# Optimization experiments

Hardware: AMD Instinct MI355X
Metric: run time of the kernel (lower is better)

The kernel has to match this reference:

```python
import jax, jax.numpy as jnp
import numpy as np

N = 100000      # nodes
E = 1600000     # edges (avg degree 16)
FEAT = 128
HID = 64
OUT = 64
NIDX = 10000
P_DROP = 0.5


def setup_inputs() -> dict:
    key = jax.random.key(0)
    ks = jax.random.split(key, 10)
    x = jax.random.normal(ks[0], (N, FEAT), jnp.float32)
    row = jax.random.randint(ks[1], (E,), 0, N)
    col = jax.random.randint(ks[2], (E,), 0, N)
    # precomputed symmetric-normalized adjacency values (D^-1/2 A D^-1/2)
    vals = jax.random.uniform(ks[3], (E,), jnp.float32) / 16.0
    W1 = jax.random.normal(ks[4], (FEAT, HID), jnp.float32) / np.sqrt(FEAT)
    b1 = jnp.zeros((HID,), jnp.float32)
    W2 = jax.random.normal(ks[5], (HID, OUT), jnp.float32) / np.sqrt(HID)
    b2 = jnp.zeros((OUT,), jnp.float32)
    # inverted-dropout mask, precomputed for determinism
    drop_mask = (jax.random.uniform(ks[6], (N, HID)) > P_DROP).astype(jnp.float32) / (1.0 - P_DROP)
    idx = jax.random.randint(ks[7], (NIDX,), 0, N)
    return dict(x=x, vals=vals, W1=W1, b1=b1, W2=W2, b2=b2,
                drop_mask=drop_mask, row=row, col=col, idx=idx)


def spmm(vals, row, col, x):
    # out[r] = sum_e vals[e] * x[col[e]] for edges with row[e]==r
    return jax.ops.segment_sum(vals[:, None] * x[col], row, num_segments=N)


def reference(x, vals, W1, b1, W2, b2, drop_mask, row, col, idx):
    h = spmm(vals, row, col, x @ W1 + b1)          # GCNConv 1: linear then A_hat @ h
    h = jax.nn.relu(h) * drop_mask                  # relu + dropout
    h = spmm(vals, row, col, h @ W2 + b2)          # GCNConv 2
    return h[idx]
```

## Files before the change

### kernel.cpp

```cpp
#include <hip/hip_runtime.h>
#include <hip/hip_bf16.h>

#define FEAT 128
#define HID  64
#define OUT  64


__global__ void scatter_direct(const int* __restrict__ row, const int* __restrict__ col,
                               const float* __restrict__ vals, int* __restrict__ cursor,
                               int2* __restrict__ edges, int E, int maxdeg) {
    int e = blockIdx.x * blockDim.x + threadIdx.x;
    if (e >= E) return;
    int r = row[e];
    int p = atomicAdd(&cursor[r], 1);
    if (p < maxdeg) {
        int2 d;
        d.x = col[e];
        d.y = __float_as_int(vals[e]);
        edges[(size_t)r * maxdeg + p] = d;
    }
}


__global__ __launch_bounds__(256) void gemm1(const float* __restrict__ x,
                                             const float* __restrict__ W1,
                                             const float* __restrict__ b1,
                                             float* __restrict__ h0, int N) {
    __shared__ float W1s[FEAT][HID];
    __shared__ float b1s[HID];
    int t = threadIdx.x;
    for (int i = t; i < FEAT * HID / 4; i += 256)
        ((float4*)&W1s[0][0])[i] = ((const float4*)W1)[i];
    if (t < HID) b1s[t] = b1[t];
    __syncthreads();

    int wave = t >> 6, lane = t & 63;
    int nquad = N >> 2;
    for (int q = blockIdx.x * 4 + wave; q < nquad; q += gridDim.x * 4) {
        int r0 = q * 4;
        const float4* x0 = (const float4*)(x + (size_t)(r0 + 0) * FEAT);
        const float4* x1 = (const float4*)(x + (size_t)(r0 + 1) * FEAT);
        const float4* x2 = (const float4*)(x + (size_t)(r0 + 2) * FEAT);
        const float4* x3 = (const float4*)(x + (size_t)(r0 + 3) * FEAT);
        float bb = b1s[lane];
        float a0 = bb, a1 = bb, a2 = bb, a3 = bb;
        #pragma unroll
        for (int k4 = 0; k4 < FEAT / 4; ++k4) {
            float w0 = W1s[k4 * 4 + 0][lane];
            float w1 = W1s[k4 * 4 + 1][lane];
            float w2 = W1s[k4 * 4 + 2][lane];
            float w3 = W1s[k4 * 4 + 3][lane];
            float4 v0 = x0[k4], v1 = x1[k4], v2 = x2[k4], v3 = x3[k4];
            a0 += v0.x * w0 + v0.y * w1 + v0.z * w2 + v0.w * w3;
            a1 += v1.x * w0 + v1.y * w1 + v1.z * w2 + v1.w * w3;
            a2 += v2.x * w0 + v2.y * w1 + v2.z * w2 + v2.w * w3;
            a3 += v3.x * w0 + v3.y * w1 + v3.z * w2 + v3.w * w3;
        }
        h0[(size_t)(r0 + 0) * HID + lane] = a0;
        h0[(size_t)(r0 + 1) * HID + lane] = a1;
        h0[(size_t)(r0 + 2) * HID + lane] = a2;
        h0[(size_t)(r0 + 3) * HID + lane] = a3;
    }
}


__device__ inline float gather_row(const float* __restrict__ feat,
                                   const int2* __restrict__ ed,
                                   int beg, int end, int lane) {
    float acc = 0.f;
    int e = beg;
    for (; e + 8 <= end; e += 8) {
        int4 p0 = *(const int4*)(ed + e);
        int4 p1 = *(const int4*)(ed + e + 2);
        int4 p2 = *(const int4*)(ed + e + 4);
        int4 p3 = *(const int4*)(ed + e + 6);
        float g0 = feat[(size_t)p0.x * HID + lane];
        float g1 = feat[(size_t)p0.z * HID + lane];
        float g2 = feat[(size_t)p1.x * HID + lane];
        float g3 = feat[(size_t)p1.z * HID + lane];
        float g4 = feat[(size_t)p2.x * HID + lane];
        float g5 = feat[(size_t)p2.z * HID + lane];
        float g6 = feat[(size_t)p3.x * HID + lane];
        float g7 = feat[(size_t)p3.z * HID + lane];
        acc += __int_as_float(p0.y) * g0; acc += __int_as_float(p0.w) * g1;
        acc += __int_as_float(p1.y) * g2; acc += __int_as_float(p1.w) * g3;
        acc += __int_as_float(p2.y) * g4; acc += __int_as_float(p2.w) * g5;
        acc += __int_as_float(p3.y) * g6; acc += __int_as_float(p3.w) * g7;
    }
    for (; e + 2 <= end; e += 2) {
        int4 p = *(const int4*)(ed + e);
        float g0 = feat[(size_t)p.x * HID + lane];
        float g1 = feat[(size_t)p.z * HID + lane];
        acc += __int_as_float(p.y) * g0; acc += __int_as_float(p.w) * g1;
    }
    if (e < end) {
        int2 p = ed[e];
        acc += __int_as_float(p.y) * feat[(size_t)p.x * HID + lane];
    }
    return acc;
}

__device__ inline float gather_row_sum(const float* __restrict__ feat,
                                       const int2* __restrict__ ed,
                                       int beg, int end, int lane, float& vsum) {
    float acc = 0.f, s = 0.f;
    int e = beg;
    for (; e + 8 <= end; e += 8) {
        int4 p0 = *(const int4*)(ed + e);
        int4 p1 = *(const int4*)(ed + e + 2);
        int4 p2 = *(const int4*)(ed + e + 4);
        int4 p3 = *(const int4*)(ed + e + 6);
        float g0 = feat[(size_t)p0.x * HID + lane];
        float g1 = feat[(size_t)p0.z * HID + lane];
        float g2 = feat[(size_t)p1.x * HID + lane];
        float g3 = feat[(size_t)p1.z * HID + lane];
        float g4 = feat[(size_t)p2.x * HID + lane];
        float g5 = feat[(size_t)p2.z * HID + lane];
        float g6 = feat[(size_t)p3.x * HID + lane];
        float g7 = feat[(size_t)p3.z * HID + lane];
        acc += __int_as_float(p0.y) * g0; acc += __int_as_float(p0.w) * g1;
        acc += __int_as_float(p1.y) * g2; acc += __int_as_float(p1.w) * g3;
        acc += __int_as_float(p2.y) * g4; acc += __int_as_float(p2.w) * g5;
        acc += __int_as_float(p3.y) * g6; acc += __int_as_float(p3.w) * g7;
        s += __int_as_float(p0.y) + __int_as_float(p0.w);
        s += __int_as_float(p1.y) + __int_as_float(p1.w);
        s += __int_as_float(p2.y) + __int_as_float(p2.w);
        s += __int_as_float(p3.y) + __int_as_float(p3.w);
    }
    for (; e + 2 <= end; e += 2) {
        int4 p = *(const int4*)(ed + e);
        float g0 = feat[(size_t)p.x * HID + lane];
        float g1 = feat[(size_t)p.z * HID + lane];
        acc += __int_as_float(p.y) * g0; acc += __int_as_float(p.w) * g1;
        s += __int_as_float(p.y) + __int_as_float(p.w);
    }
    if (e < end) {
        int2 p = ed[e];
        acc += __int_as_float(p.y) * feat[(size_t)p.x * HID + lane];
        s += __int_as_float(p.y);
    }
    vsum = s;
    return acc;
}


__global__ __launch_bounds__(256) void spmm1_relu(const float* __restrict__ h0,
                                                  const int* __restrict__ cursor,
                                                  const int2* __restrict__ edges,
                                                  const float* __restrict__ mask,
                                                  float* __restrict__ h2,
                                                  int N, int maxdeg) {
    int t = threadIdx.x, wave = t >> 6, lane = t & 63;
    for (int r = blockIdx.x * 4 + wave; r < N; r += gridDim.x * 4) {
        int deg = min(cursor[r], maxdeg);
        int beg = r * maxdeg;
        float mk = mask[(size_t)r * HID + lane];
        float acc = gather_row(h0, edges, beg, beg + deg, lane);
        h2[(size_t)r * HID + lane] = fmaxf(acc, 0.f) * mk;
    }
}


__global__ __launch_bounds__(256) void spmm2_gemm2(const float* __restrict__ h2,
                                                   const int* __restrict__ cursor,
                                                   const int2* __restrict__ edges,
                                                   const int* __restrict__ idx,
                                                   const float* __restrict__ W2,
                                                   const float* __restrict__ b2,
                                                   float* __restrict__ out,
                                                   int NIDX, int maxdeg) {
    __shared__ float W2s[HID][OUT];
    __shared__ float b2s[OUT];
    __shared__ float gs[4][HID];
    int t = threadIdx.x;
    for (int i = t; i < HID * OUT / 4; i += 256)
        ((float4*)&W2s[0][0])[i] = ((const float4*)W2)[i];
    if (t < OUT) b2s[t] = b2[t];
    __syncthreads();

    int wave = t >> 6, lane = t & 63;
    int i = blockIdx.x * 4 + wave;
    if (i >= NIDX) return;
    int r = idx[i];
    int deg = min(cursor[r], maxdeg);
    int beg = r * maxdeg;
    float vsum;
    float g = gather_row_sum(h2, edges, beg, beg + deg, lane, vsum);
    gs[wave][lane] = g;
    float o = vsum * b2s[lane];
    #pragma unroll
    for (int f = 0; f < HID; ++f)
        o += gs[wave][f] * W2s[f][lane];
    out[(size_t)i * OUT + lane] = o;
}


extern "C" void kernel_launch(void* const* d_in, const int* in_sizes, int n_in,
                              void* d_out, int out_size, void* d_ws, size_t ws_size,
                              hipStream_t stream) {
    const float* x    = (const float*)d_in[0];
    const float* vals = (const float*)d_in[1];
    const float* W1   = (const float*)d_in[2];
    const float* b1   = (const float*)d_in[3];
    const float* W2   = (const float*)d_in[4];
    const float* b2   = (const float*)d_in[5];
    const float* mask = (const float*)d_in[6];
    const int*   row  = (const int*)d_in[7];
    const int*   col  = (const int*)d_in[8];
    const int*   idx  = (const int*)d_in[9];
    float* out = (float*)d_out;

    const int N    = in_sizes[0] / FEAT;
    const int E    = in_sizes[1];
    const int NIDX = in_sizes[9];

    auto need = [&](int md) {
        return (size_t)N * HID * 4 + 256
             + (size_t)N * HID * 4 + 256
             + (size_t)N * 4 + 256
             + (size_t)N * md * 8 + 256;
    };
    int maxdeg = 48;
    while (maxdeg > 32 && need(maxdeg) > ws_size) maxdeg -= 4;

    char* ws = (char*)d_ws;
    size_t off = 0;
    auto alloc = [&](size_t bytes) { void* p = ws + off; off = (off + bytes + 255) & ~(size_t)255; return p; };
    float* h0     = (float*)alloc((size_t)N * HID * 4);
    float* h2     = (float*)alloc((size_t)N * HID * 4);
    int*   cursor = (int*)  alloc((size_t)N * 4);
    int2*  edges  = (int2*) alloc((size_t)N * maxdeg * 8);

    hipMemsetAsync(cursor, 0, (size_t)N * 4, stream);

    scatter_direct<<<(E + 255) / 256, 256, 0, stream>>>(row, col, vals, cursor, edges, E, maxdeg);
    gemm1<<<1024, 256, 0, stream>>>(x, W1, b1, h0, N);
    spmm1_relu<<<4096, 256, 0, stream>>>(h0, cursor, edges, mask, h2, N, maxdeg);
    spmm2_gemm2<<<(NIDX + 3) / 4, 256, 0, stream>>>(h2, cursor, edges, idx, W2, b2, out, NIDX, maxdeg);
}
```

Before: 408.9 us.

## Fuse edge scatter with GEMM1 and pad edge rows to process pairs of rows

Edge bucketing and the first linear layer now run in one launch, with even blocks doing the atomic scatter and odd blocks doing a shared-memory-tiled x@W1. The edge buffer is zero-filled so the SpMM loops can step in fixed groups of 8 padded edges without tail handling, and spmm1 has each wave handle two rows at once for more memory-level parallelism. This adds a memset of the whole padded edge buffer and wasted gathers on padding entries, which read node 0 with weight zero.

Measured after the change: 548.6 us. 1.34x slower.

```diff
diff --git a/kernel.cpp b/kernel.cpp
--- a/kernel.cpp
+++ b/kernel.cpp
@@ -4,143 +4,86 @@
 #define FEAT 128
 #define HID  64
 #define OUT  64
-
-
-__global__ void scatter_direct(const int* __restrict__ row, const int* __restrict__ col,
-                               const float* __restrict__ vals, int* __restrict__ cursor,
-                               int2* __restrict__ edges, int E, int maxdeg) {
-    int e = blockIdx.x * blockDim.x + threadIdx.x;
-    if (e >= E) return;
-    int r = row[e];
-    int p = atomicAdd(&cursor[r], 1);
-    if (p < maxdeg) {
-        int2 d;
-        d.x = col[e];
-        d.y = __float_as_int(vals[e]);
-        edges[(size_t)r * maxdeg + p] = d;
-    }
-}
-
-
-__global__ __launch_bounds__(256) void gemm1(const float* __restrict__ x,
-                                             const float* __restrict__ W1,
-                                             const float* __restrict__ b1,
-                                             float* __restrict__ h0, int N) {
+#define NTILE 16
+
+
+__global__ __launch_bounds__(256) void fused_scatter_gemm1(
+        const int* __restrict__ row, const int* __restrict__ col,
+        const float* __restrict__ vals, int* __restrict__ cursor,
+        int2* __restrict__ edges, int E, int maxdeg,
+        const float* __restrict__ x, const float* __restrict__ W1,
+        const float* __restrict__ b1, float* __restrict__ h0, int N,
+        int halfGrid) {
     __shared__ float W1s[FEAT][HID];
     __shared__ float b1s[HID];
+    __shared__ float xs[NTILE][FEAT];
     int t = threadIdx.x;
-    for (int i = t; i < FEAT * HID / 4; i += 256)
-        ((float4*)&W1s[0][0])[i] = ((const float4*)W1)[i];
-    if (t < HID) b1s[t] = b1[t];
-    __syncthreads();
-
-    int wave = t >> 6, lane = t & 63;
-    int nquad = N >> 2;
-    for (int q = blockIdx.x * 4 + wave; q < nquad; q += gridDim.x * 4) {
-        int r0 = q * 4;
-        const float4* x0 = (const float4*)(x + (size_t)(r0 + 0) * FEAT);
-        const float4* x1 = (const float4*)(x + (size_t)(r0 + 1) * FEAT);
-        const float4* x2 = (const float4*)(x + (size_t)(r0 + 2) * FEAT);
-        const float4* x3 = (const float4*)(x + (size_t)(r0 + 3) * FEAT);
-        float bb = b1s[lane];
-        float a0 = bb, a1 = bb, a2 = bb, a3 = bb;
-        #pragma unroll
-        for (int k4 = 0; k4 < FEAT / 4; ++k4) {
-            float w0 = W1s[k4 * 4 + 0][lane];
-            float w1 = W1s[k4 * 4 + 1][lane];
-            float w2 = W1s[k4 * 4 + 2][lane];
-            float w3 = W1s[k4 * 4 + 3][lane];
-            float4 v0 = x0[k4], v1 = x1[k4], v2 = x2[k4], v3 = x3[k4];
-            a0 += v0.x * w0 + v0.y * w1 + v0.z * w2 + v0.w * w3;
-            a1 += v1.x * w0 + v1.y * w1 + v1.z * w2 + v1.w * w3;
-            a2 += v2.x * w0 + v2.y * w1 + v2.z * w2 + v2.w * w3;
-            a3 += v3.x * w0 + v3.y * w1 + v3.z * w2 + v3.w * w3;
+    int bid = blockIdx.x;
+
+    if ((bid & 1) == 0) {
+        int tid = (bid >> 1) * 256 + t;
+        int S = halfGrid * 256;
+        int e0 = tid, e1 = tid + S, e2 = tid + 2 * S;
+        bool v0 = e0 < E, v1 = e1 < E, v2 = e2 < E;
+        int r0 = v0 ? row[e0] : 0;
+        int r1 = v1 ? row[e1] : 0;
+        int r2 = v2 ? row[e2] : 0;
+        int p0 = v0 ? atomicAdd(&cursor[r0], 1) : 0;
+        int p1 = v1 ? atomicAdd(&cursor[r1], 1) : 0;
+        int p2 = v2 ? atomicAdd(&cursor[r2], 1) : 0;
+        if (v0 && p0 < maxdeg)
+            edges[(size_t)r0 * maxdeg + p0] = make_int2(col[e0], __float_as_int(vals[e0]));
+        if (v1 && p1 < maxdeg)
+            edges[(size_t)r1 * maxdeg + p1] = make_int2(col[e1], __float_as_int(vals[e1]));
+        if (v2 && p2 < maxdeg)
+            edges[(size_t)r2 * maxdeg + p2] = make_int2(col[e2], __float_as_int(vals[e2]));
+        for (int e = tid + 3 * S; e < E; e += S) {
+            int r = row[e];
+            int p = atomicAdd(&cursor[r], 1);
+            if (p < maxdeg)
+                edges[(size_t)r * maxdeg + p] = make_int2(col[e], __float_as_int(vals[e]));
         }
-        h0[(size_t)(r0 + 0) * HID + lane] = a0;
-        h0[(size_t)(r0 + 1) * HID + lane] = a1;
-        h0[(size_t)(r0 + 2) * HID + lane] = a2;
-        h0[(size_t)(r0 + 3) * HID + lane] = a3;
+    } else {
+        for (int i = t; i < FEAT * HID / 4; i += 256)
+            ((float4*)&W1s[0][0])[i] = ((const float4*)W1)[i];
+        if (t < HID) b1s[t] = b1[t];
+        __syncthreads();
+        int wave = t >> 6, lane = t & 63;
+        int ntile = (N + NTILE - 1) / NTILE;
+        for (int tile = bid >> 1; tile < ntile; tile += halfGrid) {
+            int base = tile * NTILE;
+            float4* xs4 = (float4*)&xs[0][0];
+            const float4* xg = (const float4*)(x + (size_t)base * FEAT);
+            int lim = min(N - base, NTILE) * (FEAT / 4);
+            float4 z; z.x = z.y = z.z = z.w = 0.f;
+            xs4[t]       = (t < lim)       ? xg[t]       : z;
+            xs4[t + 256] = (t + 256 < lim) ? xg[t + 256] : z;
+            __syncthreads();
+            int r0 = base + wave * 4;
+            float bb = b1s[lane];
+            float a0 = bb, a1 = bb, a2 = bb, a3 = bb;
+            #pragma unroll
+            for (int k4 = 0; k4 < FEAT / 4; ++k4) {
+                float w0 = W1s[k4 * 4 + 0][lane];
+                float w1 = W1s[k4 * 4 + 1][lane];
+                float w2 = W1s[k4 * 4 + 2][lane];
+                float w3 = W1s[k4 * 4 + 3][lane];
+                float4 v0 = ((const float4*)xs[wave * 4 + 0])[k4];
+                float4 v1 = ((const float4*)xs[wave * 4 + 1])[k4];
+                float4 v2 = ((const float4*)xs[wave * 4 + 2])[k4];
+                float4 v3 = ((const float4*)xs[wave * 4 + 3])[k4];
+                a0 += v0.x * w0 + v0.y * w1 + v0.z * w2 + v0.w * w3;
+                a1 += v1.x * w0 + v1.y * w1 + v1.z * w2 + v1.w * w3;
+                a2 += v2.x * w0 + v2.y * w1 + v2.z * w2 + v2.w * w3;
+                a3 += v3.x * w0 + v3.y * w1 + v3.z * w2 + v3.w * w3;
+            }
+            if (r0 + 0 < N) h0[(size_t)(r0 + 0) * HID + lane] = a0;
+            if (r0 + 1 < N) h0[(size_t)(r0 + 1) * HID + lane] = a1;
+            if (r0 + 2 < N) h0[(size_t)(r0 + 2) * HID + lane] = a2;
+            if (r0 + 3 < N) h0[(size_t)(r0 + 3) * HID + lane] = a3;
+            __syncthreads();
+        }
     }
-}
-
-
-__device__ inline float gather_row(const float* __restrict__ feat,
-                                   const int2* __restrict__ ed,
-                                   int beg, int end, int lane) {
-    float acc = 0.f;
-    int e = beg;
-    for (; e + 8 <= end; e += 8) {
-        int4 p0 = *(const int4*)(ed + e);
-        int4 p1 = *(const int4*)(ed + e + 2);
-        int4 p2 = *(const int4*)(ed + e + 4);
-        int4 p3 = *(const int4*)(ed + e + 6);
-        float g0 = feat[(size_t)p0.x * HID + lane];
-        float g1 = feat[(size_t)p0.z * HID + lane];
-        float g2 = feat[(size_t)p1.x * HID + lane];
-        float g3 = feat[(size_t)p1.z * HID + lane];
-        float g4 = feat[(size_t)p2.x * HID + lane];
-        float g5 = feat[(size_t)p2.z * HID + lane];
-        float g6 = feat[(size_t)p3.x * HID + lane];
-        float g7 = feat[(size_t)p3.z * HID + lane];
-        acc += __int_as_float(p0.y) * g0; acc += __int_as_float(p0.w) * g1;
-        acc += __int_as_float(p1.y) * g2; acc += __int_as_float(p1.w) * g3;
-        acc += __int_as_float(p2.y) * g4; acc += __int_as_float(p2.w) * g5;
-        acc += __int_as_float(p3.y) * g6; acc += __int_as_float(p3.w) * g7;
-    }
-    for (; e + 2 <= end; e += 2) {
-        int4 p = *(const int4*)(ed + e);
-        float g0 = feat[(size_t)p.x * HID + lane];
-        float g1 = feat[(size_t)p.z * HID + lane];
-        acc += __int_as_float(p.y) * g0; acc += __int_as_float(p.w) * g1;
-    }
-    if (e < end) {
-        int2 p = ed[e];
-        acc += __int_as_float(p.y) * feat[(size_t)p.x * HID + lane];
-    }
-    return acc;
-}
-
-__device__ inline float gather_row_sum(const float* __restrict__ feat,
-                                       const int2* __restrict__ ed,
-                                       int beg, int end, int lane, float& vsum) {
-    float acc = 0.f, s = 0.f;
-    int e = beg;
-    for (; e + 8 <= end; e += 8) {
-        int4 p0 = *(const int4*)(ed + e);
-        int4 p1 = *(const int4*)(ed + e + 2);
-        int4 p2 = *(const int4*)(ed + e + 4);
-        int4 p3 = *(const int4*)(ed + e + 6);
-        float g0 = feat[(size_t)p0.x * HID + lane];
-        float g1 = feat[(size_t)p0.z * HID + lane];
-        float g2 = feat[(size_t)p1.x * HID + lane];
-        float g3 = feat[(size_t)p1.z * HID + lane];
-        float g4 = feat[(size_t)p2.x * HID + lane];
-        float g5 = feat[(size_t)p2.z * HID + lane];
-        float g6 = feat[(size_t)p3.x * HID + lane];
-        float g7 = feat[(size_t)p3.z * HID + lane];
-        acc += __int_as_float(p0.y) * g0; acc += __int_as_float(p0.w) * g1;
-        acc += __int_as_float(p1.y) * g2; acc += __int_as_float(p1.w) * g3;
-        acc += __int_as_float(p2.y) * g4; acc += __int_as_float(p2.w) * g5;
-        acc += __int_as_float(p3.y) * g6; acc += __int_as_float(p3.w) * g7;
-        s += __int_as_float(p0.y) + __int_as_float(p0.w);
-        s += __int_as_float(p1.y) + __int_as_float(p1.w);
-        s += __int_as_float(p2.y) + __int_as_float(p2.w);
-        s += __int_as_float(p3.y) + __int_as_float(p3.w);
-    }
-    for (; e + 2 <= end; e += 2) {
-        int4 p = *(const int4*)(ed + e);
-        float g0 = feat[(size_t)p.x * HID + lane];
-        float g1 = feat[(size_t)p.z * HID + lane];
-        acc += __int_as_float(p.y) * g0; acc += __int_as_float(p.w) * g1;
-        s += __int_as_float(p.y) + __int_as_float(p.w);
-    }
-    if (e < end) {
-        int2 p = ed[e];
-        acc += __int_as_float(p.y) * feat[(size_t)p.x * HID + lane];
-        s += __int_as_float(p.y);
-    }
-    vsum = s;
-    return acc;
 }
 
 
@@ -151,12 +94,49 @@
                                                   float* __restrict__ h2,
                                                   int N, int maxdeg) {
     int t = threadIdx.x, wave = t >> 6, lane = t & 63;
-    for (int r = blockIdx.x * 4 + wave; r < N; r += gridDim.x * 4) {
-        int deg = min(cursor[r], maxdeg);
-        int beg = r * maxdeg;
-        float mk = mask[(size_t)r * HID + lane];
-        float acc = gather_row(h0, edges, beg, beg + deg, lane);
-        h2[(size_t)r * HID + lane] = fmaxf(acc, 0.f) * mk;
+    int npair = (N + 1) >> 1;
+    for (int g = blockIdx.x * 4 + wave; g < npair; g += gridDim.x * 4) {
+        int rA = 2 * g, rB = 2 * g + 1;
+        bool vB = rB < N;
+        int degA = min(cursor[rA], maxdeg);
+        int degB = vB ? min(cursor[rB], maxdeg) : 0;
+        int nA = (degA + 7) >> 3, nB = (degB + 7) >> 3;
+        int n = max(nA, nB);
+        const int4* qA = (const int4*)(edges + (size_t)rA * maxdeg);
+        const int4* qB = (const int4*)(edges + (size_t)(vB ? rB : rA) * maxdeg);
+        float mkA = mask[(size_t)rA * HID + lane];
+        float mkB = vB ? mask[(size_t)rB * HID + lane] : 0.f;
+        float accA = 0.f, accB = 0.f;
+        for (int i = 0; i < n; ++i) {
+            int4 A0 = qA[i * 4 + 0], A1 = qA[i * 4 + 1], A2 = qA[i * 4 + 2], A3 = qA[i * 4 + 3];
+            int4 B0 = qB[i * 4 + 0], B1 = qB[i * 4 + 1], B2 = qB[i * 4 + 2], B3 = qB[i * 4 + 3];
+            float gA0 = h0[(size_t)A0.x * HID + lane];
+            float gA1 = h0[(size_t)A0.z * HID + lane];
+            float gA2 = h0[(size_t)A1.x * HID + lane];
+            float gA3 = h0[(size_t)A1.z * HID + lane];
+            float gA4 = h0[(size_t)A2.x * HID + lane];
+            float gA5 = h0[(size_t)A2.z * HID + lane];
+            float gA6 = h0[(size_t)A3.x * HID + lane];
+            float gA7 = h0[(size_t)A3.z * HID + lane];
+            float gB0 = h0[(size_t)B0.x * HID + lane];
+            float gB1 = h0[(size_t)B0.z * HID + lane];
+            float gB2 = h0[(size_t)B1.x * HID + lane];
+            float gB3 = h0[(size_t)B1.z * HID + lane];
+            float gB4 = h0[(size_t)B2.x * HID + lane];
+            float gB5 = h0[(size_t)B2.z * HID + lane];
+            float gB6 = h0[(size_t)B3.x * HID + lane];
+            float gB7 = h0[(size_t)B3.z * HID + lane];
+            accA += __int_as_float(A0.y) * gA0; accA += __int_as_float(A0.w) * gA1;
+            accA += __int_as_float(A1.y) * gA2; accA += __int_as_float(A1.w) * gA3;
+            accA += __int_as_float(A2.y) * gA4; accA += __int_as_float(A2.w) * gA5;
+            accA += __int_as_float(A3.y) * gA6; accA += __int_as_float(A3.w) * gA7;
+            accB += __int_as_float(B0.y) * gB0; accB += __int_as_float(B0.w) * gB1;
+            accB += __int_as_float(B1.y) * gB2; accB += __int_as_float(B1.w) * gB3;
+            accB += __int_as_float(B2.y) * gB4; accB += __int_as_float(B2.w) * gB5;
+            accB += __int_as_float(B3.y) * gB6; accB += __int_as_float(B3.w) * gB7;
+        }
+        h2[(size_t)rA * HID + lane] = fmaxf(accA, 0.f) * mkA;
+        if (vB) h2[(size_t)rB * HID + lane] = fmaxf(accB, 0.f) * mkB;
     }
 }
 
@@ -183,11 +163,30 @@
     if (i >= NIDX) return;
     int r = idx[i];
     int deg = min(cursor[r], maxdeg);
-    int beg = r * maxdeg;
-    float vsum;
-    float g = gather_row_sum(h2, edges, beg, beg + deg, lane, vsum);
-    gs[wave][lane] = g;
-    float o = vsum * b2s[lane];
+    int n = (deg + 7) >> 3;
+    const int4* q = (const int4*)(edges + (size_t)r * maxdeg);
+    float acc = 0.f, s = 0.f;
+    for (int k = 0; k < n; ++k) {
+        int4 p0 = q[k * 4 + 0], p1 = q[k * 4 + 1], p2 = q[k * 4 + 2], p3 = q[k * 4 + 3];
+        float g0 = h2[(size_t)p0.x * HID + lane];
+        float g1 = h2[(size_t)p0.z * HID + lane];
+        float g2 = h2[(size_t)p1.x * HID + lane];
+        float g3 = h2[(size_t)p1.z * HID + lane];
+        float g4 = h2[(size_t)p2.x * HID + lane];
+        float g5 = h2[(size_t)p2.z * HID + lane];
+        float g6 = h2[(size_t)p3.x * HID + lane];
+        float g7 = h2[(size_t)p3.z * HID + lane];
+        acc += __int_as_float(p0.y) * g0; acc += __int_as_float(p0.w) * g1;
+        acc += __int_as_float(p1.y) * g2; acc += __int_as_float(p1.w) * g3;
+        acc += __int_as_float(p2.y) * g4; acc += __int_as_float(p2.w) * g5;
+        acc += __int_as_float(p3.y) * g6; acc += __int_as_float(p3.w) * g7;
+        s += __int_as_float(p0.y) + __int_as_float(p0.w);
+        s += __int_as_float(p1.y) + __int_as_float(p1.w);
+        s += __int_as_float(p2.y) + __int_as_float(p2.w);
+        s += __int_as_float(p3.y) + __int_as_float(p3.w);
+    }
+    gs[wave][lane] = acc;
+    float o = s * b2s[lane];
     #pragma unroll
     for (int f = 0; f < HID; ++f)
         o += gs[wave][f] * W2s[f][lane];
@@ -221,7 +220,7 @@
              + (size_t)N * md * 8 + 256;
     };
     int maxdeg = 48;
-    while (maxdeg > 32 && need(maxdeg) > ws_size) maxdeg -= 4;
+    while (maxdeg > 32 && need(maxdeg) > ws_size) maxdeg -= 8;
 
     char* ws = (char*)d_ws;
     size_t off = 0;
@@ -232,9 +231,11 @@
     int2*  edges  = (int2*) alloc((size_t)N * maxdeg * 8);
 
     hipMemsetAsync(cursor, 0, (size_t)N * 4, stream);
-
-    scatter_direct<<<(E + 255) / 256, 256, 0, stream>>>(row, col, vals, cursor, edges, E, maxdeg);
-    gemm1<<<1024, 256, 0, stream>>>(x, W1, b1, h0, N);
+    hipMemsetAsync(edges, 0, (size_t)N * maxdeg * 8, stream);
+
+    const int halfGrid = 2048;
+    fused_scatter_gemm1<<<2 * halfGrid, 256, 0, stream>>>(
+        row, col, vals, cursor, edges, E, maxdeg, x, W1, b1, h0, N, halfGrid);
     spmm1_relu<<<4096, 256, 0, stream>>>(h0, cursor, edges, mask, h2, N, maxdeg);
     spmm2_gemm2<<<(NIDX + 3) / 4, 256, 0, stream>>>(h2, cursor, edges, idx, W2, b2, out, NIDX, maxdeg);
 }
```
